# Performance work log

Hardware: AMD Instinct MI355X
Metric: run time of the kernel (lower is better)

## Reference

```python
import jax, jax.numpy as jnp
import numpy as np

IN_FEATURES = 4096
OUT_FEATURES = 4096
RANK = 16
N_BITS = 4
SCALING = 0.01
QMIN = -(2 ** (N_BITS - 1))      # -8
QMAX = 2 ** (N_BITS - 1) - 1     #  7
EPS = 1e-8


@jax.custom_vjp
def ste_quant(x, scale):
    """Fake-quantize with straight-through estimator (zero_point = 0)."""
    q = jnp.clip(jnp.round(x / scale), QMIN, QMAX)
    return q * scale


def _ste_fwd(x, scale):
    return ste_quant(x, scale), (x, scale)


def _ste_bwd(res, g):
    x, scale = res
    q = x / scale
    mask = ((q >= QMIN) & (q <= QMAX)).astype(g.dtype)
    # Torch STE returns grad only for input; scale gets no gradient.
    gs = jnp.zeros(scale.shape, dtype=g.dtype)
    return (g * mask, gs)


ste_quant.defvjp(_ste_fwd, _ste_bwd)


def setup_inputs() -> dict:
    key = jax.random.key(0)
    ks = jax.random.split(key, 4)
    x = jax.random.normal(ks[0], (4, 2048, IN_FEATURES), dtype=jnp.float32)
    pretrained_weight = 0.1 * jax.random.normal(ks[1], (OUT_FEATURES, IN_FEATURES), dtype=jnp.float32)
    lora_A = np.sqrt(2.0 / RANK) * jax.random.normal(ks[2], (RANK, IN_FEATURES), dtype=jnp.float32)
    # Original inits lora_B to zeros; use small random values so the LoRA path is non-degenerate.
    lora_B = 0.01 * jax.random.normal(ks[3], (OUT_FEATURES, RANK), dtype=jnp.float32)
    # Mirror initialize_scales(): per-channel 99th-percentile |w| / 2^(n_bits-1).
    weight_max = jnp.quantile(jnp.abs(pretrained_weight), 0.99, axis=1)
    weight_scale = weight_max / (2 ** (N_BITS - 1))
    activation_scale = jnp.ones((1,), dtype=jnp.float32)
    bias = jnp.zeros((OUT_FEATURES,), dtype=jnp.float32)
    return {
        "x": x,
        "pretrained_weight": pretrained_weight,
        "lora_A": lora_A,
        "lora_B": lora_B,
        "weight_scale": weight_scale,
        "activation_scale": activation_scale,
        "bias": bias,
    }


def reference(x, pretrained_weight, lora_A, lora_B, weight_scale, activation_scale, bias):
    # LoRA merge: [out, in]
    merged = pretrained_weight + SCALING * (lora_B @ lora_A)
    wsc = jnp.maximum(jnp.abs(weight_scale), EPS)      # [out]
    asc = jnp.maximum(jnp.abs(activation_scale), EPS)  # [1]
    # Per-output-channel fake quant of the weight (vectorized over the torch loop).
    w_q = ste_quant(merged, wsc[:, None])              # [out, in]
    x_q = ste_quant(x, asc)                            # [b, s, in]
    # F.linear: x_q @ w_q^T + bias
    return jnp.einsum("bsi,oi->bso", x_q, w_q) + bias
```

## Files before the change

### kernel.cpp

```cpp
#include <hip/hip_runtime.h>
#include <cstdint>
#include <cstddef>

#define IN_F 4096
#define OUT_F 4096
#define RANKK 16
#define EPSQ 1e-8f
#define LSCALE 0.01f

typedef __attribute__((ext_vector_type(4))) int i32x4;
typedef __attribute__((ext_vector_type(16))) int i32x16;

__device__ __forceinline__ float quantf(float v, float s) {
    float q = rintf(v / s);
    return fminf(7.f, fmaxf(-8.f, q));
}

__global__ __launch_bounds__(256) void qx_kernel(const float* __restrict__ x,
                                                 const float* __restrict__ ascale,
                                                 int8_t* __restrict__ qx) {
    const float asc = fmaxf(fabsf(ascale[0]), EPSQ);
    const int i = blockIdx.x * 256 + threadIdx.x;
    float4 v = ((const float4*)x)[i];
    union { int8_t b[4]; int w; } u;
    u.b[0] = (int8_t)(int)quantf(v.x, asc);
    u.b[1] = (int8_t)(int)quantf(v.y, asc);
    u.b[2] = (int8_t)(int)quantf(v.z, asc);
    u.b[3] = (int8_t)(int)quantf(v.w, asc);
    ((int*)qx)[i] = u.w;
}

__global__ __launch_bounds__(256) void qw_kernel(const float* __restrict__ W,
                                                 const float* __restrict__ lA,
                                                 const float* __restrict__ lB,
                                                 const float* __restrict__ wscale,
                                                 int8_t* __restrict__ qw) {
    __shared__ float Ablk[RANKK][256];
    __shared__ float Bblk[64][RANKK];
    const int tid = threadIdx.x;
    const int i0 = blockIdx.x * 256;
    const int o0 = blockIdx.y * 64;

#pragma unroll
    for (int r = 0; r < RANKK; ++r)
        Ablk[r][tid] = lA[r * IN_F + i0 + tid];
    for (int j = tid; j < 64 * RANKK; j += 256)
        Bblk[j >> 4][j & 15] = lB[(size_t)(o0 + (j >> 4)) * RANKK + (j & 15)];
    __syncthreads();

    const int i = i0 + tid;
    for (int o = 0; o < 64; ++o) {
        float s = 0.f;
#pragma unroll
        for (int r = 0; r < RANKK; ++r) s += Bblk[o][r] * Ablk[r][tid];
        float merged = W[(size_t)(o0 + o) * IN_F + i] + LSCALE * s;
        float wsc = fmaxf(fabsf(wscale[o0 + o]), EPSQ);
        qw[(size_t)(o0 + o) * IN_F + i] = (int8_t)(int)quantf(merged, wsc);
    }
}

constexpr int BM = 128, BN = 128, BK = 64, KD = 4096;

__global__ __launch_bounds__(256) void gemm_i8_kernel(
        const int8_t* __restrict__ qx, const int8_t* __restrict__ qw,
        const float* __restrict__ wscale, const float* __restrict__ ascale,
        const float* __restrict__ bias, float* __restrict__ out) {
    __shared__ __attribute__((aligned(16))) int8_t As[BM * BK];
    __shared__ __attribute__((aligned(16))) int8_t Bs[BN * BK];

    const int tid  = threadIdx.x;
    const int lane = tid & 63;
    const int wave = tid >> 6;
    const int m_tile = blockIdx.y * BM;
    const int n_tile = blockIdx.x * BN;
    const int wm = (wave >> 1) * 64;
    const int wn = (wave & 1) * 64;

    int stage_off[2];
#pragma unroll
    for (int is = 0; is < 2; ++is) {
        int p = wave * 128 + is * 64 + lane;
        int m = p >> 2;
        int q = (p & 3) ^ ((m >> 1) & 3);
        stage_off[is] = m * KD + q * 16;
    }
    const int8_t* Abase = qx + (size_t)m_tile * KD;
    const int8_t* Bbase = qw + (size_t)n_tile * KD;

    int rdA[2][2], rdB[2][2];
#pragma unroll
    for (int mi = 0; mi < 2; ++mi) {
        const int ra = wm + mi * 32 + (lane & 31);
        const int rb = wn + mi * 32 + (lane & 31);
#pragma unroll
        for (int kk = 0; kk < 2; ++kk) {
            const int qn = kk * 2 + (lane >> 5);
            rdA[mi][kk] = ra * 64 + ((qn ^ ((ra >> 1) & 3)) * 16);
            rdB[mi][kk] = rb * 64 + ((qn ^ ((rb >> 1) & 3)) * 16);
        }
    }

    i32x16 acc[2][2];
#pragma unroll
    for (int mi = 0; mi < 2; ++mi)
#pragma unroll
        for (int ni = 0; ni < 2; ++ni) acc[mi][ni] = (i32x16)(0);

    for (int k0 = 0; k0 < KD; k0 += BK) {
#pragma unroll
        for (int is = 0; is < 2; ++is) {
            __builtin_amdgcn_global_load_lds(
                (const __attribute__((address_space(1))) void*)(Abase + k0 + stage_off[is]),
                (__attribute__((address_space(3))) void*)(As + wave * 2048 + is * 1024),
                16, 0, 0);
            __builtin_amdgcn_global_load_lds(
                (const __attribute__((address_space(1))) void*)(Bbase + k0 + stage_off[is]),
                (__attribute__((address_space(3))) void*)(Bs + wave * 2048 + is * 1024),
                16, 0, 0);
        }
        __syncthreads();
#pragma unroll
        for (int kk = 0; kk < 2; ++kk) {
            i32x4 af[2], bf[2];
#pragma unroll
            for (int mi = 0; mi < 2; ++mi) af[mi] = *(const i32x4*)(As + rdA[mi][kk]);
#pragma unroll
            for (int ni = 0; ni < 2; ++ni) bf[ni] = *(const i32x4*)(Bs + rdB[ni][kk]);
#pragma unroll
            for (int mi = 0; mi < 2; ++mi)
#pragma unroll
                for (int ni = 0; ni < 2; ++ni)
                    acc[mi][ni] = __builtin_amdgcn_mfma_i32_32x32x32_i8(
                        af[mi], bf[ni], acc[mi][ni], 0, 0, 0);
        }
        __syncthreads();
    }

    const float asc = fmaxf(fabsf(ascale[0]), EPSQ);
#pragma unroll
    for (int ni = 0; ni < 2; ++ni) {
        const int n  = n_tile + wn + ni * 32 + (lane & 31);
        const float sc = asc * fmaxf(fabsf(wscale[n]), EPSQ);
        const float bb = bias[n];
#pragma unroll
        for (int mi = 0; mi < 2; ++mi) {
            const int rbase = m_tile + wm + mi * 32 + 4 * (lane >> 5);
#pragma unroll
            for (int r = 0; r < 16; ++r) {
                const int row = rbase + (r & 3) + 8 * (r >> 2);
                out[(size_t)row * OUT_F + n] = sc * (float)acc[mi][ni][r] + bb;
            }
        }
    }
}

extern "C" void kernel_launch(void* const* d_in, const int* in_sizes, int n_in,
                              void* d_out, int out_size, void* d_ws, size_t ws_size,
                              hipStream_t stream) {
    const float* x      = (const float*)d_in[0];
    const float* W      = (const float*)d_in[1];
    const float* lA     = (const float*)d_in[2];
    const float* lB     = (const float*)d_in[3];
    const float* wscale = (const float*)d_in[4];
    const float* ascale = (const float*)d_in[5];
    const float* bias   = (const float*)d_in[6];
    float* out = (float*)d_out;

    const int M = in_sizes[0] / IN_F;
    int8_t* qx = (int8_t*)d_ws;
    int8_t* qw = qx + (size_t)M * IN_F;

    qx_kernel<<<(in_sizes[0] / 4 + 255) / 256, 256, 0, stream>>>(x, ascale, qx);
    qw_kernel<<<dim3(IN_F / 256, OUT_F / 64), 256, 0, stream>>>(W, lA, lB, wscale, qw);
    gemm_i8_kernel<<<dim3(OUT_F / BN, M / BM), 256, 0, stream>>>(
        qx, qw, wscale, ascale, bias, out);
}
```

Before: 441.7 us.

## Widen int8 GEMM tile to 128x256 with new LDS swizzle and staging

Doubles the N tile of the int8 MFMA GEMM so each wave computes a 64x128 output block with eight accumulators, increasing reuse of A fragments loaded from LDS and halving A global reloads. The global-to-LDS staging is reorganized so all threads cooperatively load contiguous row chunks, using a different XOR swizzle mask to avoid bank conflicts. It also adds a two-blocks-per-CU launch bound and partial unrolling in the weight quantization loop. The larger tile raises register and LDS pressure and halves the number of blocks, which may reduce occupancy or load balance.

```diff
diff --git a/kernel.cpp b/kernel.cpp
--- a/kernel.cpp
+++ b/kernel.cpp
@@ -14,6 +14,10 @@
 __device__ __forceinline__ float quantf(float v, float s) {
     float q = rintf(v / s);
     return fminf(7.f, fmaxf(-8.f, q));
+}
+
+__device__ __forceinline__ int swzmask(int m) {
+    return (((m >> 1) & 1) << 1) | ((m >> 2) & 1);
 }
 
 __global__ __launch_bounds__(256) void qx_kernel(const float* __restrict__ x,
@@ -49,6 +53,7 @@
     __syncthreads();
 
     const int i = i0 + tid;
+#pragma unroll 4
     for (int o = 0; o < 64; ++o) {
         float s = 0.f;
 #pragma unroll
@@ -59,9 +64,9 @@
     }
 }
 
-constexpr int BM = 128, BN = 128, BK = 64, KD = 4096;
+constexpr int BM = 128, BN = 256, BK = 64, KD = 4096;
 
-__global__ __launch_bounds__(256) void gemm_i8_kernel(
+__global__ __launch_bounds__(256, 2) void gemm_i8_kernel(
         const int8_t* __restrict__ qx, const int8_t* __restrict__ qw,
         const float* __restrict__ wscale, const float* __restrict__ ascale,
         const float* __restrict__ bias, float* __restrict__ out) {
@@ -71,65 +76,78 @@
     const int tid  = threadIdx.x;
     const int lane = tid & 63;
     const int wave = tid >> 6;
+    const int hi   = lane >> 5;
     const int m_tile = blockIdx.y * BM;
     const int n_tile = blockIdx.x * BN;
     const int wm = (wave >> 1) * 64;
-    const int wn = (wave & 1) * 64;
+    const int wn = (wave & 1) * 128;
 
-    int stage_off[2];
+    int srcA[2], srcB[4];
 #pragma unroll
     for (int is = 0; is < 2; ++is) {
-        int p = wave * 128 + is * 64 + lane;
+        int p = is * 256 + tid;
         int m = p >> 2;
-        int q = (p & 3) ^ ((m >> 1) & 3);
-        stage_off[is] = m * KD + q * 16;
+        int q = (p & 3) ^ swzmask(m);
+        srcA[is] = m * KD + q * 16;
+    }
+#pragma unroll
+    for (int is = 0; is < 4; ++is) {
+        int p = is * 256 + tid;
+        int m = p >> 2;
+        int q = (p & 3) ^ swzmask(m);
+        srcB[is] = m * KD + q * 16;
     }
     const int8_t* Abase = qx + (size_t)m_tile * KD;
     const int8_t* Bbase = qw + (size_t)n_tile * KD;
 
-    int rdA[2][2], rdB[2][2];
+    int baseA[2], maskA[2], baseB[4], maskB[4];
 #pragma unroll
     for (int mi = 0; mi < 2; ++mi) {
         const int ra = wm + mi * 32 + (lane & 31);
-        const int rb = wn + mi * 32 + (lane & 31);
+        baseA[mi] = ra * 64;
+        maskA[mi] = swzmask(ra);
+    }
 #pragma unroll
-        for (int kk = 0; kk < 2; ++kk) {
-            const int qn = kk * 2 + (lane >> 5);
-            rdA[mi][kk] = ra * 64 + ((qn ^ ((ra >> 1) & 3)) * 16);
-            rdB[mi][kk] = rb * 64 + ((qn ^ ((rb >> 1) & 3)) * 16);
-        }
+    for (int ni = 0; ni < 4; ++ni) {
+        const int rb = wn + ni * 32 + (lane & 31);
+        baseB[ni] = rb * 64;
+        maskB[ni] = swzmask(rb);
     }
 
-    i32x16 acc[2][2];
+    i32x16 acc[2][4];
 #pragma unroll
     for (int mi = 0; mi < 2; ++mi)
 #pragma unroll
-        for (int ni = 0; ni < 2; ++ni) acc[mi][ni] = (i32x16)(0);
+        for (int ni = 0; ni < 4; ++ni) acc[mi][ni] = (i32x16)(0);
 
     for (int k0 = 0; k0 < KD; k0 += BK) {
 #pragma unroll
-        for (int is = 0; is < 2; ++is) {
+        for (int is = 0; is < 2; ++is)
             __builtin_amdgcn_global_load_lds(
-                (const __attribute__((address_space(1))) void*)(Abase + k0 + stage_off[is]),
-                (__attribute__((address_space(3))) void*)(As + wave * 2048 + is * 1024),
+                (const __attribute__((address_space(1))) void*)(Abase + k0 + srcA[is]),
+                (__attribute__((address_space(3))) void*)(As + (is * 256 + wave * 64) * 16),
                 16, 0, 0);
+#pragma unroll
+        for (int is = 0; is < 4; ++is)
             __builtin_amdgcn_global_load_lds(
-                (const __attribute__((address_space(1))) void*)(Bbase + k0 + stage_off[is]),
-                (__attribute__((address_space(3))) void*)(Bs + wave * 2048 + is * 1024),
+                (const __attribute__((address_space(1))) void*)(Bbase + k0 + srcB[is]),
+                (__attribute__((address_space(3))) void*)(Bs + (is * 256 + wave * 64) * 16),
                 16, 0, 0);
-        }
         __syncthreads();
 #pragma unroll
         for (int kk = 0; kk < 2; ++kk) {
-            i32x4 af[2], bf[2];
+            const int q = kk * 2 + hi;
+            i32x4 af[2], bf[4];
 #pragma unroll
-            for (int mi = 0; mi < 2; ++mi) af[mi] = *(const i32x4*)(As + rdA[mi][kk]);
+            for (int mi = 0; mi < 2; ++mi)
+                af[mi] = *(const i32x4*)(As + baseA[mi] + ((q ^ maskA[mi]) * 16));
 #pragma unroll
-            for (int ni = 0; ni < 2; ++ni) bf[ni] = *(const i32x4*)(Bs + rdB[ni][kk]);
+            for (int ni = 0; ni < 4; ++ni)
+                bf[ni] = *(const i32x4*)(Bs + baseB[ni] + ((q ^ maskB[ni]) * 16));
 #pragma unroll
             for (int mi = 0; mi < 2; ++mi)
 #pragma unroll
-                for (int ni = 0; ni < 2; ++ni)
+                for (int ni = 0; ni < 4; ++ni)
                     acc[mi][ni] = __builtin_amdgcn_mfma_i32_32x32x32_i8(
                         af[mi], bf[ni], acc[mi][ni], 0, 0, 0);
         }
@@ -138,13 +156,13 @@
 
     const float asc = fmaxf(fabsf(ascale[0]), EPSQ);
 #pragma unroll
-    for (int ni = 0; ni < 2; ++ni) {
+    for (int ni = 0; ni < 4; ++ni) {
         const int n  = n_tile + wn + ni * 32 + (lane & 31);
         const float sc = asc * fmaxf(fabsf(wscale[n]), EPSQ);
         const float bb = bias[n];
 #pragma unroll
         for (int mi = 0; mi < 2; ++mi) {
-            const int rbase = m_tile + wm + mi * 32 + 4 * (lane >> 5);
+            const int rbase = m_tile + wm + mi * 32 + 4 * hi;
 #pragma unroll
             for (int r = 0; r < 16; ++r) {
                 const int row = rbase + (r & 3) + 8 * (r >> 2);
```

Result: faster. 430.0 us (-2.6%).
